# Optimization experiments

Measured on AMD Instinct MI355X. Metric: run time of the kernel, lower is better.

The kernel has to match this reference:

```python
import jax, jax.numpy as jnp
import numpy as np

E, NG, NM, H = 260640, 65160, 40962, 256


def _layer_norm(x, g, b, eps=1e-5):
    mu = jnp.mean(x, axis=-1, keepdims=True)
    var = jnp.mean(jnp.square(x - mu), axis=-1, keepdims=True)
    return (x - mu) * jax.lax.rsqrt(var + eps) * g + b


def _mlp(x, W1, b1, W2, b2, g, b):
    # Linear -> SiLU -> Linear -> LayerNorm (MLP with n_layers=1)
    h = jax.nn.silu(x @ W1 + b1)
    return _layer_norm(h @ W2 + b2, g, b)


def _lin(key, fan_in, fan_out):
    kw, kb = jax.random.split(key)
    s = 1.0 / np.sqrt(fan_in)
    W = jax.random.uniform(kw, (fan_in, fan_out), jnp.float32, -s, s)
    bb = jax.random.uniform(kb, (fan_out,), jnp.float32, -s, s)
    return W, bb


def setup_inputs() -> dict:
    key = jax.random.key(0)
    ks = jax.random.split(key, 12)
    inp = {
        'g2m_efeat': jax.random.normal(ks[0], (E, H), jnp.float32),
        'grid_feat': jax.random.normal(ks[1], (NG, H), jnp.float32),
        'mesh_feat': jax.random.normal(ks[2], (NM, H), jnp.float32),
        'src_idx': jax.random.randint(ks[3], (E,), 0, NG),
        'dst_idx': jax.random.randint(ks[4], (E,), 0, NM),
    }
    # edge MLP: in = 3H (efeat + src + dst)
    inp['eW1'], inp['eb1'] = _lin(ks[5], 3 * H, H)
    inp['eW2'], inp['eb2'] = _lin(ks[6], H, H)
    inp['eg'], inp['ebt'] = jnp.ones((H,), jnp.float32), jnp.zeros((H,), jnp.float32)
    # src (grid) node MLP: in = H
    inp['sW1'], inp['sb1'] = _lin(ks[7], H, H)
    inp['sW2'], inp['sb2'] = _lin(ks[8], H, H)
    inp['sg'], inp['sbt'] = jnp.ones((H,), jnp.float32), jnp.zeros((H,), jnp.float32)
    # dst (mesh) node MLP: in = 2H (agg + mesh)
    inp['dW1'], inp['db1'] = _lin(ks[9], 2 * H, H)
    inp['dW2'], inp['db2'] = _lin(ks[10], H, H)
    inp['dg'], inp['dbt'] = jnp.ones((H,), jnp.float32), jnp.zeros((H,), jnp.float32)
    return inp


def reference(g2m_efeat, grid_feat, mesh_feat, src_idx, dst_idx,
              eW1, eb1, eW2, eb2, eg, ebt,
              sW1, sb1, sW2, sb2, sg, sbt,
              dW1, db1, dW2, db2, dg, dbt):
    # gather src/dst node features and concat with edge features  [E, 3H]
    cat = jnp.concatenate([g2m_efeat, grid_feat[src_idx], mesh_feat[dst_idx]], axis=-1)
    efeat = _mlp(cat, eW1, eb1, eW2, eb2, eg, ebt)  # [E, H]
    # scatter-sum edges to mesh (dst) nodes, concat with mesh feats
    agg = jax.ops.segment_sum(efeat, dst_idx, num_segments=mesh_feat.shape[0])  # [NM, H]
    mesh_new = mesh_feat + _mlp(jnp.concatenate([agg, mesh_feat], axis=-1),
                                dW1, db1, dW2, db2, dg, dbt)
    grid_new = grid_feat + _mlp(grid_feat, sW1, sb1, sW2, sb2, sg, sbt)
    return (grid_new, mesh_new)
```

## Files before the change

### kernel.cpp

```cpp
#include <hip/hip_runtime.h>

#define Hdim 256
static const int E_N  = 260640;
static const int NG_N = 65160;
static const int NM_N = 40962;

typedef __attribute__((ext_vector_type(8))) __bf16 bf16x8;
typedef __attribute__((ext_vector_type(8))) unsigned short u16x8;
typedef __attribute__((ext_vector_type(4))) float f32x4;

__device__ __forceinline__ unsigned short f2bf(float f) {
  unsigned u = __float_as_uint(f);
  u = (u + 0x7FFFu + ((u >> 16) & 1u)) >> 16;
  return (unsigned short)u;
}
__device__ __forceinline__ float bf2f(unsigned short h) {
  return __uint_as_float((unsigned)h << 16);
}
struct BfPair { unsigned short hi, lo; };
__device__ __forceinline__ BfPair split2(float f) {
  BfPair r;
  r.hi = f2bf(f);
  r.lo = f2bf(f - bf2f(r.hi));
  return r;
}
__device__ __forceinline__ BfPair split2t(float f) {
  unsigned u = __float_as_uint(f);
  BfPair r;
  r.hi = (unsigned short)(u >> 16);
  r.lo = f2bf(f - __uint_as_float(u & 0xffff0000u));
  return r;
}
__device__ __forceinline__ int hswz(int row) {
  return ((row & 7) << 3) ^ (((row >> 2) & 3) << 4);
}
__device__ __forceinline__ void bar_lds() {
  asm volatile("s_waitcnt lgkmcnt(0)" ::: "memory");
  __builtin_amdgcn_s_barrier();
}

__global__ void wfrag_kernel(const float* __restrict__ W,
                             unsigned short* __restrict__ Fh,
                             unsigned short* __restrict__ Fl, int K, int N) {
  int i = blockIdx.x * 256 + threadIdx.x;
  if (i >= K * N) return;
  int k = i / N;
  int col = i - k * N;
  BfPair p = split2(W[i]);
  int t = k >> 5, rem = k & 31;
  int lg = rem >> 3, j = rem & 7;
  int cb = col >> 4, lr = col & 15;
  long o = ((long)(t * 16 + cb) * 64 + (lg * 16 + lr)) * 8 + j;
  Fh[o] = p.hi;
  Fl[o] = p.lo;
}

template <bool A3>
struct SMem {
  union {
    unsigned short ahi[2][64][72];
    float lnp[4][64][2];
  } u;
  unsigned short alo[A3 ? 2 : 1][A3 ? 64 : 1][A3 ? 72 : 1];
  unsigned short hh[64 * 256];
};

template <int NSEG, bool SCATTER, bool A3>
__launch_bounds__(256, 2)
__global__ void mlp_mfma(
    const float* s0, const float* s1, const float* s2,
    const int* __restrict__ i1, const int* __restrict__ i2, int M,
    const unsigned short* __restrict__ W1Fh, const unsigned short* __restrict__ W1Fl,
    const float* __restrict__ b1,
    const unsigned short* __restrict__ W2Fh, const unsigned short* __restrict__ W2Fl,
    const float* __restrict__ b2,
    const float* __restrict__ gamma, const float* __restrict__ beta,
    const float* residual, float* outp,
    float* agg, const int* __restrict__ scat) {
  constexpr int K1 = NSEG * 256;
  constexpr int NT = K1 / 32;
  constexpr int NU = K1 / 64;
  __shared__ SMem<A3> sm;

  const int tid = threadIdx.x;
  const int w = tid >> 6;
  const int l = tid & 63;
  const int lr = l & 15;
  const int lg = l >> 4;
  const int colbase = w * 64 + lr;
  const long blockRow = (long)blockIdx.x * 64;

  const long grow_s = blockRow + l;
  const long growc = grow_s < M ? grow_s : (long)(M - 1);
  const float* rp0 = s0 + growc * Hdim;
  const float* rp1 = nullptr;
  const float* rp2 = nullptr;
  if (NSEG >= 2) rp1 = s1 + (long)(i1 ? i1[growc] : (int)growc) * Hdim;
  if (NSEG >= 3) rp2 = s2 + (long)(i2 ? i2[growc] : (int)growc) * Hdim;

  auto aptr = [&](int m) -> const float* {
    const int seg = m >> 2;
    const float* rp = rp0;
    if (NSEG >= 2 && seg == 1) rp = rp1;
    if (NSEG >= 3 && seg == 2) rp = rp2;
    return rp + (m & 3) * 64 + w * 16;
  };

  auto loadA = [&](int m, float4* v) {
    const float* p = aptr(m);
#pragma unroll
    for (int i = 0; i < 4; ++i) v[i] = *(const float4*)(p + i * 4);
  };

  auto stageA = [&](int buf, const float4* v) {
    float in[16] = {v[0].x, v[0].y, v[0].z, v[0].w, v[1].x, v[1].y, v[1].z, v[1].w,
                    v[2].x, v[2].y, v[2].z, v[2].w, v[3].x, v[3].y, v[3].z, v[3].w};
    if constexpr (A3) {
      u16x8 th0, tl0, th1, tl1;
#pragma unroll
      for (int j = 0; j < 8; ++j) {
        BfPair p0 = split2t(in[j]);
        th0[j] = p0.hi; tl0[j] = p0.lo;
        BfPair p1 = split2t(in[j + 8]);
        th1[j] = p1.hi; tl1[j] = p1.lo;
      }
      *(u16x8*)&sm.u.ahi[buf][l][w * 16]     = th0;
      *(u16x8*)&sm.u.ahi[buf][l][w * 16 + 8] = th1;
      *(u16x8*)&sm.alo[buf][l][w * 16]       = tl0;
      *(u16x8*)&sm.alo[buf][l][w * 16 + 8]   = tl1;
    } else {
      u16x8 th0, th1;
#pragma unroll
      for (int j = 0; j < 8; ++j) {
        th0[j] = f2bf(in[j]);
        th1[j] = f2bf(in[j + 8]);
      }
      *(u16x8*)&sm.u.ahi[buf][l][w * 16]     = th0;
      *(u16x8*)&sm.u.ahi[buf][l][w * 16 + 8] = th1;
    }
  };

  auto loadB1 = [&](int t, bf16x8* bh, bf16x8* bl) {
#pragma unroll
    for (int n = 0; n < 4; ++n) {
      const long o = ((long)(t * 16 + w * 4 + n) * 64 + l) * 8;
      bh[n] = *(const bf16x8*)(W1Fh + o);
      bl[n] = *(const bf16x8*)(W1Fl + o);
    }
  };

  f32x4 acc[4][4] = {};
  {
    float4 v[4];
    loadA(0, v);
    stageA(0, v);
  }
  float4 va[4], vb[4];
  loadA(1 < NU ? 1 : NU - 1, va);
  bf16x8 bhc[4], blc[4];
  loadB1(0, bhc, blc);

  for (int u = 0; u < NU; ++u) {
    bar_lds();
    loadA(u + 2 < NU ? u + 2 : NU - 1, vb);
    bf16x8 bhn[4], bln[4];
    loadB1(2 * u + 1 < NT ? 2 * u + 1 : NT - 1, bhn, bln);
    bf16x8 ah[4], al[4];
#pragma unroll
    for (int rb = 0; rb < 4; ++rb) {
      ah[rb] = *(const bf16x8*)&sm.u.ahi[u & 1][rb * 16 + lr][lg * 8];
      if constexpr (A3) al[rb] = *(const bf16x8*)&sm.alo[u & 1][rb * 16 + lr][lg * 8];
    }
    __builtin_amdgcn_s_setprio(1);
#pragma unroll
    for (int rb = 0; rb < 4; ++rb)
#pragma unroll
      for (int n = 0; n < 4; ++n) {
        acc[rb][n] = __builtin_amdgcn_mfma_f32_16x16x32_bf16(ah[rb], bhc[n], acc[rb][n], 0, 0, 0);
        acc[rb][n] = __builtin_amdgcn_mfma_f32_16x16x32_bf16(ah[rb], blc[n], acc[rb][n], 0, 0, 0);
        if constexpr (A3)
          acc[rb][n] = __builtin_amdgcn_mfma_f32_16x16x32_bf16(al[rb], bhc[n], acc[rb][n], 0, 0, 0);
      }
    __builtin_amdgcn_s_setprio(0);
    bf16x8 bh2[4], bl2[4];
    loadB1(2 * u + 2 < NT ? 2 * u + 2 : NT - 1, bh2, bl2);
#pragma unroll
    for (int rb = 0; rb < 4; ++rb) {
      ah[rb] = *(const bf16x8*)&sm.u.ahi[u & 1][rb * 16 + lr][32 + lg * 8];
      if constexpr (A3) al[rb] = *(const bf16x8*)&sm.alo[u & 1][rb * 16 + lr][32 + lg * 8];
    }
    __builtin_amdgcn_s_setprio(1);
#pragma unroll
    for (int rb = 0; rb < 4; ++rb)
#pragma unroll
      for (int n = 0; n < 4; ++n) {
        acc[rb][n] = __builtin_amdgcn_mfma_f32_16x16x32_bf16(ah[rb], bhn[n], acc[rb][n], 0, 0, 0);
        acc[rb][n] = __builtin_amdgcn_mfma_f32_16x16x32_bf16(ah[rb], bln[n], acc[rb][n], 0, 0, 0);
        if constexpr (A3)
          acc[rb][n] = __builtin_amdgcn_mfma_f32_16x16x32_bf16(al[rb], bhn[n], acc[rb][n], 0, 0, 0);
      }
    __builtin_amdgcn_s_setprio(0);
    if (u + 1 < NU) stageA((u + 1) & 1, va);
#pragma unroll
    for (int i = 0; i < 4; ++i) va[i] = vb[i];
#pragma unroll
    for (int n = 0; n < 4; ++n) { bhc[n] = bh2[n]; blc[n] = bl2[n]; }
  }

  bf16x8 b2hc[4], b2lc[4];
#pragma unroll
  for (int n = 0; n < 4; ++n) {
    const long o = ((long)(w * 4 + n) * 64 + l) * 8;
    b2hc[n] = *(const bf16x8*)(W2Fh + o);
    b2lc[n] = *(const bf16x8*)(W2Fl + o);
  }

  float bb1[4];
#pragma unroll
  for (int n = 0; n < 4; ++n) bb1[n] = b1[colbase + n * 16];
#pragma unroll
  for (int rb = 0; rb < 4; ++rb) {
#pragma unroll
    for (int n = 0; n < 4; ++n) {
      const int col = colbase + n * 16;
#pragma unroll
      for (int r = 0; r < 4; ++r) {
        const int row = rb * 16 + lg * 4 + r;
        float v = acc[rb][n][r] + bb1[n];
        v = v / (1.0f + __expf(-v));
        sm.hh[row * 256 + (col ^ hswz(row))] = f2bf(v);
      }
    }
  }
  bar_lds();

  f32x4 acc2[4][4] = {};
  for (int ks = 0; ks < 8; ++ks) {
    const int kn = (ks + 1 < 8) ? ks + 1 : ks;
    bf16x8 b2hn[4], b2ln[4];
#pragma unroll
    for (int n = 0; n < 4; ++n) {
      const long o = ((long)(kn * 16 + w * 4 + n) * 64 + l) * 8;
      b2hn[n] = *(const bf16x8*)(W2Fh + o);
      b2ln[n] = *(const bf16x8*)(W2Fl + o);
    }
    bf16x8 ah[4];
#pragma unroll
    for (int rb = 0; rb < 4; ++rb) {
      const int row = rb * 16 + lr;
      ah[rb] = *(const bf16x8*)&sm.hh[row * 256 + ((ks * 32 + lg * 8) ^ hswz(row))];
    }
    __builtin_amdgcn_s_setprio(1);
#pragma unroll
    for (int rb = 0; rb < 4; ++rb)
#pragma unroll
      for (int n = 0; n < 4; ++n) {
        acc2[rb][n] = __builtin_amdgcn_mfma_f32_16x16x32_bf16(ah[rb], b2hc[n], acc2[rb][n], 0, 0, 0);
        acc2[rb][n] = __builtin_amdgcn_mfma_f32_16x16x32_bf16(ah[rb], b2lc[n], acc2[rb][n], 0, 0, 0);
      }
    __builtin_amdgcn_s_setprio(0);
#pragma unroll
    for (int n = 0; n < 4; ++n) { b2hc[n] = b2hn[n]; b2lc[n] = b2ln[n]; }
  }
  __syncthreads();

  float bb2[4], gmv[4], btv[4];
#pragma unroll
  for (int n = 0; n < 4; ++n) {
    const int c = colbase + n * 16;
    bb2[n] = b2[c];
    gmv[n] = gamma[c];
    btv[n] = beta[c];
  }
  float psum[16];
#pragma unroll
  for (int rb = 0; rb < 4; ++rb)
#pragma unroll
    for (int r = 0; r < 4; ++r) {
      float s = 0.f;
#pragma unroll
      for (int n = 0; n < 4; ++n) s += acc2[rb][n][r] + bb2[n];
      psum[rb * 4 + r] = s;
    }
#pragma unroll
  for (int i = 0; i < 16; ++i) {
    psum[i] += __shfl_xor(psum[i], 1, 64);
    psum[i] += __shfl_xor(psum[i], 2, 64);
    psum[i] += __shfl_xor(psum[i], 4, 64);
    psum[i] += __shfl_xor(psum[i], 8, 64);
  }
  if (lr == 0) {
#pragma unroll
    for (int rb = 0; rb < 4; ++rb)
#pragma unroll
      for (int r = 0; r < 4; ++r)
        sm.u.lnp[w][rb * 16 + lg * 4 + r][0] = psum[rb * 4 + r];
  }
  __syncthreads();
  float mu[16];
#pragma unroll
  for (int rb = 0; rb < 4; ++rb)
#pragma unroll
    for (int r = 0; r < 4; ++r) {
      const int row = rb * 16 + lg * 4 + r;
      mu[rb * 4 + r] = (sm.u.lnp[0][row][0] + sm.u.lnp[1][row][0] +
                        sm.u.lnp[2][row][0] + sm.u.lnp[3][row][0]) * (1.0f / 256.0f);
    }
  float psq[16];
#pragma unroll
  for (int rb = 0; rb < 4; ++rb)
#pragma unroll
    for (int r = 0; r < 4; ++r) {
      float s = 0.f;
#pragma unroll
      for (int n = 0; n < 4; ++n) {
        const float d = acc2[rb][n][r] + bb2[n] - mu[rb * 4 + r];
        s += d * d;
      }
      psq[rb * 4 + r] = s;
    }
#pragma unroll
  for (int i = 0; i < 16; ++i) {
    psq[i] += __shfl_xor(psq[i], 1, 64);
    psq[i] += __shfl_xor(psq[i], 2, 64);
    psq[i] += __shfl_xor(psq[i], 4, 64);
    psq[i] += __shfl_xor(psq[i], 8, 64);
  }
  if (lr == 0) {
#pragma unroll
    for (int rb = 0; rb < 4; ++rb)
#pragma unroll
      for (int r = 0; r < 4; ++r)
        sm.u.lnp[w][rb * 16 + lg * 4 + r][1] = psq[rb * 4 + r];
  }
  __syncthreads();
#pragma unroll
  for (int rb = 0; rb < 4; ++rb) {
#pragma unroll
    for (int r = 0; r < 4; ++r) {
      const int row = rb * 16 + lg * 4 + r;
      const long grow = blockRow + row;
      if (grow >= M) continue;
      const float var = (sm.u.lnp[0][row][1] + sm.u.lnp[1][row][1] +
                         sm.u.lnp[2][row][1] + sm.u.lnp[3][row][1]) * (1.0f / 256.0f);
      const float rstd = 1.0f / sqrtf(var + 1e-5f);
      const float m = mu[rb * 4 + r];
      if constexpr (SCATTER) {
        const int d = scat[grow];
        float* ap = agg + (long)d * Hdim;
#pragma unroll
        for (int n = 0; n < 4; ++n) {
          const int c = colbase + n * 16;
          atomicAdd(ap + c, (acc2[rb][n][r] + bb2[n] - m) * rstd * gmv[n] + btv[n]);
        }
      } else {
        const long o = grow * Hdim;
#pragma unroll
        for (int n = 0; n < 4; ++n) {
          const int c = colbase + n * 16;
          outp[o + c] = (acc2[rb][n][r] + bb2[n] - m) * rstd * gmv[n] + btv[n] + residual[o + c];
        }
      }
    }
  }
}

extern "C" void kernel_launch(void* const* d_in, const int* in_sizes, int n_in,
                              void* d_out, int out_size, void* d_ws, size_t ws_size,
                              hipStream_t stream) {
  const float* g2m   = (const float*)d_in[0];
  const float* gridf = (const float*)d_in[1];
  const float* meshf = (const float*)d_in[2];
  const int*   src   = (const int*)d_in[3];
  const int*   dst   = (const int*)d_in[4];
  const float* eW1 = (const float*)d_in[5];  const float* eb1 = (const float*)d_in[6];
  const float* eW2 = (const float*)d_in[7];  const float* eb2 = (const float*)d_in[8];
  const float* eg  = (const float*)d_in[9];  const float* ebt = (const float*)d_in[10];
  const float* sW1 = (const float*)d_in[11]; const float* sb1 = (const float*)d_in[12];
  const float* sW2 = (const float*)d_in[13]; const float* sb2 = (const float*)d_in[14];
  const float* sg  = (const float*)d_in[15]; const float* sbt = (const float*)d_in[16];
  const float* dW1 = (const float*)d_in[17]; const float* db1 = (const float*)d_in[18];
  const float* dW2 = (const float*)d_in[19]; const float* db2 = (const float*)d_in[20];
  const float* dg  = (const float*)d_in[21]; const float* dbt = (const float*)d_in[22];

  float* out_grid = (float*)d_out;
  float* out_mesh = out_grid + (long)NG_N * Hdim;

  unsigned short* p = (unsigned short*)d_ws;
  unsigned short* eW1Fh = p; p += 768 * 256;  unsigned short* eW1Fl = p; p += 768 * 256;
  unsigned short* eW2Fh = p; p += 256 * 256;  unsigned short* eW2Fl = p; p += 256 * 256;
  unsigned short* sW1Fh = p; p += 256 * 256;  unsigned short* sW1Fl = p; p += 256 * 256;
  unsigned short* sW2Fh = p; p += 256 * 256;  unsigned short* sW2Fl = p; p += 256 * 256;
  unsigned short* dW1Fh = p; p += 512 * 256;  unsigned short* dW1Fl = p; p += 512 * 256;
  unsigned short* dW2Fh = p; p += 256 * 256;  unsigned short* dW2Fl = p; p += 256 * 256;

  auto WF = [&](const float* W, unsigned short* Fh, unsigned short* Fl, int K, int N) {
    int tot = K * N;
    wfrag_kernel<<<(tot + 255) / 256, 256, 0, stream>>>(W, Fh, Fl, K, N);
  };
  WF(eW1, eW1Fh, eW1Fl, 768, 256);
  WF(eW2, eW2Fh, eW2Fl, 256, 256);
  WF(sW1, sW1Fh, sW1Fl, 256, 256);
  WF(sW2, sW2Fh, sW2Fl, 256, 256);
  WF(dW1, dW1Fh, dW1Fl, 512, 256);
  WF(dW2, dW2Fh, dW2Fl, 256, 256);

  (void)hipMemsetAsync(out_mesh, 0, (size_t)NM_N * Hdim * sizeof(float), stream);

  mlp_mfma<3, true, false><<<(E_N + 63) / 64, 256, 0, stream>>>(
      g2m, gridf, meshf, src, dst, E_N,
      eW1Fh, eW1Fl, eb1, eW2Fh, eW2Fl, eb2, eg, ebt,
      nullptr, nullptr, out_mesh, dst);

  mlp_mfma<1, false, true><<<(NG_N + 63) / 64, 256, 0, stream>>>(
      gridf, nullptr, nullptr, nullptr, nullptr, NG_N,
      sW1Fh, sW1Fl, sb1, sW2Fh, sW2Fl, sb2, sg, sbt,
      gridf, out_grid, nullptr, nullptr);

  mlp_mfma<2, false, true><<<(NM_N + 63) / 64, 256, 0, stream>>>(
      out_mesh, meshf, nullptr, nullptr, nullptr, NM_N,
      dW1Fh, dW1Fl, db1, dW2Fh, dW2Fl, db2, dg, dbt,
      meshf, out_mesh, nullptr, nullptr);
}
```

Measured before the change: 752.9 us.

## Split MLP block across eight waves with half the output columns each

Raises the block from 256 to 512 threads so each of eight waves computes 32 output columns instead of 64, halving per-wave accumulator and B-fragment registers. A-tile staging is spread over eight waves and the LayerNorm partial sums now reduce over eight wave slots. This is meant to raise waves per CU and improve latency hiding. In exchange, each wave rereads the full A fragments from LDS for half the MFMA work, and barriers now synchronise more waves.

```diff
diff --git a/kernel.cpp b/kernel.cpp
--- a/kernel.cpp
+++ b/kernel.cpp
@@ -59,14 +59,14 @@
 struct SMem {
   union {
     unsigned short ahi[2][64][72];
-    float lnp[4][64][2];
+    float lnp[8][64][2];
   } u;
   unsigned short alo[A3 ? 2 : 1][A3 ? 64 : 1][A3 ? 72 : 1];
   unsigned short hh[64 * 256];
 };
 
 template <int NSEG, bool SCATTER, bool A3>
-__launch_bounds__(256, 2)
+__launch_bounds__(512, 2)
 __global__ void mlp_mfma(
     const float* s0, const float* s1, const float* s2,
     const int* __restrict__ i1, const int* __restrict__ i2, int M,
@@ -87,7 +87,7 @@
   const int l = tid & 63;
   const int lr = l & 15;
   const int lg = l >> 4;
-  const int colbase = w * 64 + lr;
+  const int colbase = w * 32 + lr;
   const long blockRow = (long)blockIdx.x * 64;
 
   const long grow_s = blockRow + l;
@@ -103,67 +103,58 @@
     const float* rp = rp0;
     if (NSEG >= 2 && seg == 1) rp = rp1;
     if (NSEG >= 3 && seg == 2) rp = rp2;
-    return rp + (m & 3) * 64 + w * 16;
+    return rp + (m & 3) * 64 + w * 8;
   };
 
   auto loadA = [&](int m, float4* v) {
     const float* p = aptr(m);
-#pragma unroll
-    for (int i = 0; i < 4; ++i) v[i] = *(const float4*)(p + i * 4);
+    v[0] = *(const float4*)p;
+    v[1] = *(const float4*)(p + 4);
   };
 
   auto stageA = [&](int buf, const float4* v) {
-    float in[16] = {v[0].x, v[0].y, v[0].z, v[0].w, v[1].x, v[1].y, v[1].z, v[1].w,
-                    v[2].x, v[2].y, v[2].z, v[2].w, v[3].x, v[3].y, v[3].z, v[3].w};
+    float in[8] = {v[0].x, v[0].y, v[0].z, v[0].w, v[1].x, v[1].y, v[1].z, v[1].w};
     if constexpr (A3) {
-      u16x8 th0, tl0, th1, tl1;
+      u16x8 th, tl;
 #pragma unroll
       for (int j = 0; j < 8; ++j) {
         BfPair p0 = split2t(in[j]);
-        th0[j] = p0.hi; tl0[j] = p0.lo;
-        BfPair p1 = split2t(in[j + 8]);
-        th1[j] = p1.hi; tl1[j] = p1.lo;
-      }
-      *(u16x8*)&sm.u.ahi[buf][l][w * 16]     = th0;
-      *(u16x8*)&sm.u.ahi[buf][l][w * 16 + 8] = th1;
-      *(u16x8*)&sm.alo[buf][l][w * 16]       = tl0;
-      *(u16x8*)&sm.alo[buf][l][w * 16 + 8]   = tl1;
+        th[j] = p0.hi; tl[j] = p0.lo;
+      }
+      *(u16x8*)&sm.u.ahi[buf][l][w * 8] = th;
+      *(u16x8*)&sm.alo[buf][l][w * 8]   = tl;
     } else {
-      u16x8 th0, th1;
-#pragma unroll
-      for (int j = 0; j < 8; ++j) {
-        th0[j] = f2bf(in[j]);
-        th1[j] = f2bf(in[j + 8]);
-      }
-      *(u16x8*)&sm.u.ahi[buf][l][w * 16]     = th0;
-      *(u16x8*)&sm.u.ahi[buf][l][w * 16 + 8] = th1;
+      u16x8 th;
+#pragma unroll
+      for (int j = 0; j < 8; ++j) th[j] = f2bf(in[j]);
+      *(u16x8*)&sm.u.ahi[buf][l][w * 8] = th;
     }
   };
 
   auto loadB1 = [&](int t, bf16x8* bh, bf16x8* bl) {
 #pragma unroll
-    for (int n = 0; n < 4; ++n) {
-      const long o = ((long)(t * 16 + w * 4 + n) * 64 + l) * 8;
+    for (int n = 0; n < 2; ++n) {
+      const long o = ((long)(t * 16 + w * 2 + n) * 64 + l) * 8;
       bh[n] = *(const bf16x8*)(W1Fh + o);
       bl[n] = *(const bf16x8*)(W1Fl + o);
     }
   };
 
-  f32x4 acc[4][4] = {};
+  f32x4 acc[4][2] = {};
   {
-    float4 v[4];
+    float4 v[2];
     loadA(0, v);
     stageA(0, v);
   }
-  float4 va[4], vb[4];
+  float4 va[2], vb[2];
   loadA(1 < NU ? 1 : NU - 1, va);
-  bf16x8 bhc[4], blc[4];
+  bf16x8 bhc[2], blc[2];
   loadB1(0, bhc, blc);
 
   for (int u = 0; u < NU; ++u) {
     bar_lds();
     loadA(u + 2 < NU ? u + 2 : NU - 1, vb);
-    bf16x8 bhn[4], bln[4];
+    bf16x8 bhn[2], bln[2];
     loadB1(2 * u + 1 < NT ? 2 * u + 1 : NT - 1, bhn, bln);
     bf16x8 ah[4], al[4];
 #pragma unroll
@@ -175,14 +166,14 @@
 #pragma unroll
     for (int rb = 0; rb < 4; ++rb)
 #pragma unroll
-      for (int n = 0; n < 4; ++n) {
+      for (int n = 0; n < 2; ++n) {
         acc[rb][n] = __builtin_amdgcn_mfma_f32_16x16x32_bf16(ah[rb], bhc[n], acc[rb][n], 0, 0, 0);
         acc[rb][n] = __builtin_amdgcn_mfma_f32_16x16x32_bf16(ah[rb], blc[n], acc[rb][n], 0, 0, 0);
         if constexpr (A3)
           acc[rb][n] = __builtin_amdgcn_mfma_f32_16x16x32_bf16(al[rb], bhc[n], acc[rb][n], 0, 0, 0);
       }
     __builtin_amdgcn_s_setprio(0);
-    bf16x8 bh2[4], bl2[4];
+    bf16x8 bh2[2], bl2[2];
     loadB1(2 * u + 2 < NT ? 2 * u + 2 : NT - 1, bh2, bl2);
 #pragma unroll
     for (int rb = 0; rb < 4; ++rb) {
@@ -193,7 +184,7 @@
 #pragma unroll
     for (int rb = 0; rb < 4; ++rb)
 #pragma unroll
-      for (int n = 0; n < 4; ++n) {
+      for (int n = 0; n < 2; ++n) {
         acc[rb][n] = __builtin_amdgcn_mfma_f32_16x16x32_bf16(ah[rb], bhn[n], acc[rb][n], 0, 0, 0);
         acc[rb][n] = __builtin_amdgcn_mfma_f32_16x16x32_bf16(ah[rb], bln[n], acc[rb][n], 0, 0, 0);
         if constexpr (A3)
@@ -202,26 +193,26 @@
     __builtin_amdgcn_s_setprio(0);
     if (u + 1 < NU) stageA((u + 1) & 1, va);
 #pragma unroll
-    for (int i = 0; i < 4; ++i) va[i] = vb[i];
-#pragma unroll
-    for (int n = 0; n < 4; ++n) { bhc[n] = bh2[n]; blc[n] = bl2[n]; }
-  }
-
-  bf16x8 b2hc[4], b2lc[4];
-#pragma unroll
-  for (int n = 0; n < 4; ++n) {
-    const long o = ((long)(w * 4 + n) * 64 + l) * 8;
+    for (int i = 0; i < 2; ++i) va[i] = vb[i];
+#pragma unroll
+    for (int n = 0; n < 2; ++n) { bhc[n] = bh2[n]; blc[n] = bl2[n]; }
+  }
+
+  bf16x8 b2hc[2], b2lc[2];
+#pragma unroll
+  for (int n = 0; n < 2; ++n) {
+    const long o = ((long)(w * 2 + n) * 64 + l) * 8;
     b2hc[n] = *(const bf16x8*)(W2Fh + o);
     b2lc[n] = *(const bf16x8*)(W2Fl + o);
   }
 
-  float bb1[4];
-#pragma unroll
-  for (int n = 0; n < 4; ++n) bb1[n] = b1[colbase + n * 16];
+  float bb1[2];
+#pragma unroll
+  for (int n = 0; n < 2; ++n) bb1[n] = b1[colbase + n * 16];
 #pragma unroll
   for (int rb = 0; rb < 4; ++rb) {
 #pragma unroll
-    for (int n = 0; n < 4; ++n) {
+    for (int n = 0; n < 2; ++n) {
       const int col = colbase + n * 16;
 #pragma unroll
       for (int r = 0; r < 4; ++r) {
@@ -234,13 +225,13 @@
   }
   bar_lds();
 
-  f32x4 acc2[4][4] = {};
+  f32x4 acc2[4][2] = {};
   for (int ks = 0; ks < 8; ++ks) {
     const int kn = (ks + 1 < 8) ? ks + 1 : ks;
-    bf16x8 b2hn[4], b2ln[4];
-#pragma unroll
-    for (int n = 0; n < 4; ++n) {
-      const long o = ((long)(kn * 16 + w * 4 + n) * 64 + l) * 8;
+    bf16x8 b2hn[2], b2ln[2];
+#pragma unroll
+    for (int n = 0; n < 2; ++n) {
+      const long o = ((long)(kn * 16 + w * 2 + n) * 64 + l) * 8;
       b2hn[n] = *(const bf16x8*)(W2Fh + o);
       b2ln[n] = *(const bf16x8*)(W2Fl + o);
     }
@@ -254,19 +245,19 @@
 #pragma unroll
     for (int rb = 0; rb < 4; ++rb)
 #pragma unroll
-      for (int n = 0; n < 4; ++n) {
+      for (int n = 0; n < 2; ++n) {
         acc2[rb][n] = __builtin_amdgcn_mfma_f32_16x16x32_bf16(ah[rb], b2hc[n], acc2[rb][n], 0, 0, 0);
         acc2[rb][n] = __builtin_amdgcn_mfma_f32_16x16x32_bf16(ah[rb], b2lc[n], acc2[rb][n], 0, 0, 0);
       }
     __builtin_amdgcn_s_setprio(0);
 #pragma unroll
-    for (int n = 0; n < 4; ++n) { b2hc[n] = b2hn[n]; b2lc[n] = b2ln[n]; }
+    for (int n = 0; n < 2; ++n) { b2hc[n] = b2hn[n]; b2lc[n] = b2ln[n]; }
   }
   __syncthreads();
 
-  float bb2[4], gmv[4], btv[4];
-#pragma unroll
-  for (int n = 0; n < 4; ++n) {
+  float bb2[2], gmv[2], btv[2];
+#pragma unroll
+  for (int n = 0; n < 2; ++n) {
     const int c = colbase + n * 16;
     bb2[n] = b2[c];
     gmv[n] = gamma[c];
@@ -279,7 +270,7 @@
     for (int r = 0; r < 4; ++r) {
       float s = 0.f;
 #pragma unroll
-      for (int n = 0; n < 4; ++n) s += acc2[rb][n][r] + bb2[n];
+      for (int n = 0; n < 2; ++n) s += acc2[rb][n][r] + bb2[n];
       psum[rb * 4 + r] = s;
     }
 #pragma unroll
@@ -303,8 +294,10 @@
 #pragma unroll
     for (int r = 0; r < 4; ++r) {
       const int row = rb * 16 + lg * 4 + r;
-      mu[rb * 4 + r] = (sm.u.lnp[0][row][0] + sm.u.lnp[1][row][0] +
-                        sm.u.lnp[2][row][0] + sm.u.lnp[3][row][0]) * (1.0f / 256.0f);
+      float s = 0.f;
+#pragma unroll
+      for (int q = 0; q < 8; ++q) s += sm.u.lnp[q][row][0];
+      mu[rb * 4 + r] = s * (1.0f / 256.0f);
     }
   float psq[16];
 #pragma unroll
@@ -313,7 +306,7 @@
     for (int r = 0; r < 4; ++r) {
       float s = 0.f;
 #pragma unroll
-      for (int n = 0; n < 4; ++n) {
+      for (int n = 0; n < 2; ++n) {
         const float d = acc2[rb][n][r] + bb2[n] - mu[rb * 4 + r];
         s += d * d;
       }
@@ -341,22 +334,24 @@
       const int row = rb * 16 + lg * 4 + r;
       const long grow = blockRow + row;
       if (grow >= M) continue;
-      const float var = (sm.u.lnp[0][row][1] + sm.u.lnp[1][row][1] +
-                         sm.u.lnp[2][row][1] + sm.u.lnp[3][row][1]) * (1.0f / 256.0f);
+      float sq = 0.f;
+#pragma unroll
+      for (int q = 0; q < 8; ++q) sq += sm.u.lnp[q][row][1];
+      const float var = sq * (1.0f / 256.0f);
       const float rstd = 1.0f / sqrtf(var + 1e-5f);
       const float m = mu[rb * 4 + r];
       if constexpr (SCATTER) {
         const int d = scat[grow];
         float* ap = agg + (long)d * Hdim;
 #pragma unroll
-        for (int n = 0; n < 4; ++n) {
+        for (int n = 0; n < 2; ++n) {
           const int c = colbase + n * 16;
           atomicAdd(ap + c, (acc2[rb][n][r] + bb2[n] - m) * rstd * gmv[n] + btv[n]);
         }
       } else {
         const long o = grow * Hdim;
 #pragma unroll
-        for (int n = 0; n < 4; ++n) {
+        for (int n = 0; n < 2; ++n) {
           const int c = colbase + n * 16;
           outp[o + c] = (acc2[rb][n][r] + bb2[n] - m) * rstd * gmv[n] + btv[n] + residual[o + c];
         }
@@ -407,17 +402,17 @@
 
   (void)hipMemsetAsync(out_mesh, 0, (size_t)NM_N * Hdim * sizeof(float), stream);
 
-  mlp_mfma<3, true, false><<<(E_N + 63) / 64, 256, 0, stream>>>(
+  mlp_mfma<3, true, false><<<(E_N + 63) / 64, 512, 0, stream>>>(
       g2m, gridf, meshf, src, dst, E_N,
       eW1Fh, eW1Fl, eb1, eW2Fh, eW2Fl, eb2, eg, ebt,
       nullptr, nullptr, out_mesh, dst);
 
-  mlp_mfma<1, false, true><<<(NG_N + 63) / 64, 256, 0, stream>>>(
+  mlp_mfma<1, false, true><<<(NG_N + 63) / 64, 512, 0, stream>>>(
       gridf, nullptr, nullptr, nullptr, nullptr, NG_N,
       sW1Fh, sW1Fl, sb1, sW2Fh, sW2Fl, sb2, sg, sbt,
       gridf, out_grid, nullptr, nullptr);
 
-  mlp_mfma<2, false, true><<<(NM_N + 63) / 64, 256, 0, stream>>>(
+  mlp_mfma<2, false, true><<<(NM_N + 63) / 64, 512, 0, stream>>>(
       out_mesh, meshf, nullptr, nullptr, nullptr, NM_N,
       dW1Fh, dW1Fl, db1, dW2Fh, dW2Fl, db2, dg, dbt,
       meshf, out_mesh, nullptr, nullptr);
```

New measurement: 982.9 us (median of 2 runs). 1.31x slower.

## Split edge MLP into gather-to-bf16-fragment pass and 128-row register-fed GEMM kernel

Applied to the files above, without the earlier changes.

The edge MLP is split into two kernels. The first gathers the concatenated edge/src/dst features, converts them to bf16, and writes them to a workspace buffer already laid out in MFMA fragment order. The second kernel uses 512 threads on 128-row tiles and loads A fragments straight from global memory into registers, skipping LDS staging and per-iteration barriers in the first GEMM. The cost is an extra round trip of roughly 400MB of bf16 through global memory, along with larger register use per thread.

```diff
diff --git a/kernel.cpp b/kernel.cpp
--- a/kernel.cpp
+++ b/kernel.cpp
@@ -4,6 +4,9 @@
 static const int E_N  = 260640;
 static const int NG_N = 65160;
 static const int NM_N = 40962;
+static const int NB_E = (E_N + 127) / 128;
+static const int RT_N = NB_E * 8;
+static const int GB_N = RT_N / 4;
 
 typedef __attribute__((ext_vector_type(8))) __bf16 bf16x8;
 typedef __attribute__((ext_vector_type(8))) unsigned short u16x8;
@@ -55,32 +58,290 @@
   Fl[o] = p.lo;
 }
 
+__global__ __launch_bounds__(256, 4)
+void gather_frag(const float* __restrict__ g2m, const float* __restrict__ gridf,
+                 const float* __restrict__ meshf, const int* __restrict__ src,
+                 const int* __restrict__ dst, int M,
+                 unsigned short* __restrict__ catF) {
+  __shared__ unsigned short tile[64][72];
+  const int tid = threadIdx.x;
+  const int w = tid >> 6;
+  const int l = tid & 63;
+  const int lr = l & 15;
+  const int lg = l >> 4;
+  const long blockRow = (long)blockIdx.x * 64;
+  long growc = blockRow + l;
+  if (growc >= M) growc = M - 1;
+  const float* rp0 = g2m + growc * Hdim;
+  const float* rp1 = gridf + (long)src[growc] * Hdim;
+  const float* rp2 = meshf + (long)dst[growc] * Hdim;
+
+  for (int m = 0; m < 12; ++m) {
+    const int seg = m >> 2;
+    const float* rp = seg == 0 ? rp0 : (seg == 1 ? rp1 : rp2);
+    const float* p = rp + (m & 3) * 64 + w * 16;
+    float4 v0 = *(const float4*)p;
+    float4 v1 = *(const float4*)(p + 4);
+    float4 v2 = *(const float4*)(p + 8);
+    float4 v3 = *(const float4*)(p + 12);
+    __syncthreads();
+    {
+      float in[16] = {v0.x, v0.y, v0.z, v0.w, v1.x, v1.y, v1.z, v1.w,
+                      v2.x, v2.y, v2.z, v2.w, v3.x, v3.y, v3.z, v3.w};
+      u16x8 t0, t1;
+#pragma unroll
+      for (int j = 0; j < 8; ++j) {
+        t0[j] = f2bf(in[j]);
+        t1[j] = f2bf(in[j + 8]);
+      }
+      *(u16x8*)&tile[l][w * 16]     = t0;
+      *(u16x8*)&tile[l][w * 16 + 8] = t1;
+    }
+    __syncthreads();
+    const long rowtile = (long)blockIdx.x * 4 + w;
+#pragma unroll
+    for (int tt = 0; tt < 2; ++tt) {
+      const int t = m * 2 + tt;
+      u16x8 v = *(const u16x8*)&tile[w * 16 + lr][tt * 32 + lg * 8];
+      *(u16x8*)&catF[((rowtile * 24 + t) * 64 + l) * 8] = v;
+    }
+  }
+}
+
+struct ESMem {
+  unsigned short hh[128 * 256];
+  float lnp[8][128][2];
+};
+
+__global__ __launch_bounds__(512, 2)
+void edge_gemm(const unsigned short* __restrict__ catF, int M,
+               const unsigned short* __restrict__ W1Fh, const unsigned short* __restrict__ W1Fl,
+               const float* __restrict__ b1,
+               const unsigned short* __restrict__ W2Fh, const unsigned short* __restrict__ W2Fl,
+               const float* __restrict__ b2,
+               const float* __restrict__ gamma, const float* __restrict__ beta,
+               float* __restrict__ agg, const int* __restrict__ scat) {
+  __shared__ ESMem sm;
+  const int tid = threadIdx.x;
+  const int w = tid >> 6;
+  const int l = tid & 63;
+  const int lr = l & 15;
+  const int lg = l >> 4;
+  const int colbase = w * 32 + lr;
+  const long blockRow = (long)blockIdx.x * 128;
+  const long rt0 = (long)blockIdx.x * 8;
+
+  auto loadAF = [&](int t, bf16x8* af) {
+#pragma unroll
+    for (int rb = 0; rb < 8; ++rb)
+      af[rb] = *(const bf16x8*)(catF + (((rt0 + rb) * 24 + t) * 64 + l) * 8);
+  };
+  auto loadB1 = [&](int t, bf16x8* bh, bf16x8* bl) {
+#pragma unroll
+    for (int n = 0; n < 2; ++n) {
+      const long o = ((long)(t * 16 + w * 2 + n) * 64 + l) * 8;
+      bh[n] = *(const bf16x8*)(W1Fh + o);
+      bl[n] = *(const bf16x8*)(W1Fl + o);
+    }
+  };
+
+  f32x4 acc[8][2] = {};
+  bf16x8 afc[8], afn[8], bhc[2], blc[2], bhn[2], bln[2];
+  loadAF(0, afc);
+  loadB1(0, bhc, blc);
+  for (int t = 0; t < 24; ++t) {
+    const int tn = t + 1 < 24 ? t + 1 : 23;
+    loadAF(tn, afn);
+    loadB1(tn, bhn, bln);
+    __builtin_amdgcn_s_setprio(1);
+#pragma unroll
+    for (int rb = 0; rb < 8; ++rb)
+#pragma unroll
+      for (int n = 0; n < 2; ++n) {
+        acc[rb][n] = __builtin_amdgcn_mfma_f32_16x16x32_bf16(afc[rb], bhc[n], acc[rb][n], 0, 0, 0);
+        acc[rb][n] = __builtin_amdgcn_mfma_f32_16x16x32_bf16(afc[rb], blc[n], acc[rb][n], 0, 0, 0);
+      }
+    __builtin_amdgcn_s_setprio(0);
+#pragma unroll
+    for (int rb = 0; rb < 8; ++rb) afc[rb] = afn[rb];
+#pragma unroll
+    for (int n = 0; n < 2; ++n) { bhc[n] = bhn[n]; blc[n] = bln[n]; }
+  }
+
+  bf16x8 b2hc[2], b2lc[2];
+#pragma unroll
+  for (int n = 0; n < 2; ++n) {
+    const long o = ((long)(w * 2 + n) * 64 + l) * 8;
+    b2hc[n] = *(const bf16x8*)(W2Fh + o);
+    b2lc[n] = *(const bf16x8*)(W2Fl + o);
+  }
+
+  float bb1[2];
+#pragma unroll
+  for (int n = 0; n < 2; ++n) bb1[n] = b1[colbase + n * 16];
+#pragma unroll
+  for (int rb = 0; rb < 8; ++rb) {
+#pragma unroll
+    for (int n = 0; n < 2; ++n) {
+      const int col = colbase + n * 16;
+#pragma unroll
+      for (int r = 0; r < 4; ++r) {
+        const int row = rb * 16 + lg * 4 + r;
+        float v = acc[rb][n][r] + bb1[n];
+        v = v / (1.0f + __expf(-v));
+        sm.hh[row * 256 + (col ^ hswz(row))] = f2bf(v);
+      }
+    }
+  }
+  bar_lds();
+
+  f32x4 acc2[8][2] = {};
+  for (int ks = 0; ks < 8; ++ks) {
+    const int kn = (ks + 1 < 8) ? ks + 1 : ks;
+    bf16x8 b2hn[2], b2ln[2];
+#pragma unroll
+    for (int n = 0; n < 2; ++n) {
+      const long o = ((long)(kn * 16 + w * 2 + n) * 64 + l) * 8;
+      b2hn[n] = *(const bf16x8*)(W2Fh + o);
+      b2ln[n] = *(const bf16x8*)(W2Fl + o);
+    }
+    __builtin_amdgcn_s_setprio(1);
+#pragma unroll
+    for (int rb = 0; rb < 8; ++rb) {
+      const int row = rb * 16 + lr;
+      bf16x8 ah = *(const bf16x8*)&sm.hh[row * 256 + ((ks * 32 + lg * 8) ^ hswz(row))];
+#pragma unroll
+      for (int n = 0; n < 2; ++n) {
+        acc2[rb][n] = __builtin_amdgcn_mfma_f32_16x16x32_bf16(ah, b2hc[n], acc2[rb][n], 0, 0, 0);
+        acc2[rb][n] = __builtin_amdgcn_mfma_f32_16x16x32_bf16(ah, b2lc[n], acc2[rb][n], 0, 0, 0);
+      }
+    }
+    __builtin_amdgcn_s_setprio(0);
+#pragma unroll
+    for (int n = 0; n < 2; ++n) { b2hc[n] = b2hn[n]; b2lc[n] = b2ln[n]; }
+  }
+
+  float bb2[2], gmv[2], btv[2];
+#pragma unroll
+  for (int n = 0; n < 2; ++n) {
+    const int c = colbase + n * 16;
+    bb2[n] = b2[c];
+    gmv[n] = gamma[c];
+    btv[n] = beta[c];
+  }
+  float psum[32];
+#pragma unroll
+  for (int rb = 0; rb < 8; ++rb)
+#pragma unroll
+    for (int r = 0; r < 4; ++r) {
+      float s = 0.f;
+#pragma unroll
+      for (int n = 0; n < 2; ++n) s += acc2[rb][n][r] + bb2[n];
+      psum[rb * 4 + r] = s;
+    }
+#pragma unroll
+  for (int i = 0; i < 32; ++i) {
+    psum[i] += __shfl_xor(psum[i], 1, 64);
+    psum[i] += __shfl_xor(psum[i], 2, 64);
+    psum[i] += __shfl_xor(psum[i], 4, 64);
+    psum[i] += __shfl_xor(psum[i], 8, 64);
+  }
+  if (lr == 0) {
+#pragma unroll
+    for (int rb = 0; rb < 8; ++rb)
+#pragma unroll
+      for (int r = 0; r < 4; ++r)
+        sm.lnp[w][rb * 16 + lg * 4 + r][0] = psum[rb * 4 + r];
+  }
+  __syncthreads();
+  float mu[32];
+#pragma unroll
+  for (int rb = 0; rb < 8; ++rb)
+#pragma unroll
+    for (int r = 0; r < 4; ++r) {
+      const int row = rb * 16 + lg * 4 + r;
+      float s = 0.f;
+#pragma unroll
+      for (int q = 0; q < 8; ++q) s += sm.lnp[q][row][0];
+      mu[rb * 4 + r] = s * (1.0f / 256.0f);
+    }
+  float psq[32];
+#pragma unroll
+  for (int rb = 0; rb < 8; ++rb)
+#pragma unroll
+    for (int r = 0; r < 4; ++r) {
+      float s = 0.f;
+#pragma unroll
+      for (int n = 0; n < 2; ++n) {
+        const float d = acc2[rb][n][r] + bb2[n] - mu[rb * 4 + r];
+        s += d * d;
+      }
+      psq[rb * 4 + r] = s;
+    }
+#pragma unroll
+  for (int i = 0; i < 32; ++i) {
+    psq[i] += __shfl_xor(psq[i], 1, 64);
+    psq[i] += __shfl_xor(psq[i], 2, 64);
+    psq[i] += __shfl_xor(psq[i], 4, 64);
+    psq[i] += __shfl_xor(psq[i], 8, 64);
+  }
+  if (lr == 0) {
+#pragma unroll
+    for (int rb = 0; rb < 8; ++rb)
+#pragma unroll
+      for (int r = 0; r < 4; ++r)
+        sm.lnp[w][rb * 16 + lg * 4 + r][1] = psq[rb * 4 + r];
+  }
+  __syncthreads();
+#pragma unroll
+  for (int rb = 0; rb < 8; ++rb) {
+#pragma unroll
+    for (int r = 0; r < 4; ++r) {
+      const int row = rb * 16 + lg * 4 + r;
+      const long grow = blockRow + row;
+      if (grow >= M) continue;
+      float sq = 0.f;
+#pragma unroll
+      for (int q = 0; q < 8; ++q) sq += sm.lnp[q][row][1];
+      const float var = sq * (1.0f / 256.0f);
+      const float rstd = 1.0f / sqrtf(var + 1e-5f);
+      const float m = mu[rb * 4 + r];
+      const int d = scat[grow];
+      float* ap = agg + (long)d * Hdim;
+#pragma unroll
+      for (int n = 0; n < 2; ++n) {
+        const int c = colbase + n * 16;
+        atomicAdd(ap + c, (acc2[rb][n][r] + bb2[n] - m) * rstd * gmv[n] + btv[n]);
+      }
+    }
+  }
+}
+
 template <bool A3>
 struct SMem {
   union {
     unsigned short ahi[2][64][72];
     float lnp[4][64][2];
   } u;
-  unsigned short alo[A3 ? 2 : 1][A3 ? 64 : 1][A3 ? 72 : 1];
+  unsigned short alo[2][64][72];
   unsigned short hh[64 * 256];
 };
 
-template <int NSEG, bool SCATTER, bool A3>
+template <int NSEG>
 __launch_bounds__(256, 2)
 __global__ void mlp_mfma(
-    const float* s0, const float* s1, const float* s2,
-    const int* __restrict__ i1, const int* __restrict__ i2, int M,
+    const float* s0, const float* s1,
+    const int* __restrict__ i1, int M,
     const unsigned short* __restrict__ W1Fh, const unsigned short* __restrict__ W1Fl,
     const float* __restrict__ b1,
     const unsigned short* __restrict__ W2Fh, const unsigned short* __restrict__ W2Fl,
     const float* __restrict__ b2,
     const float* __restrict__ gamma, const float* __restrict__ beta,
-    const float* residual, float* outp,
-    float* agg, const int* __restrict__ scat) {
+    const float* residual, float* outp) {
   constexpr int K1 = NSEG * 256;
   constexpr int NT = K1 / 32;
   constexpr int NU = K1 / 64;
-  __shared__ SMem<A3> sm;
+  __shared__ SMem<true> sm;
 
   const int tid = threadIdx.x;
   const int w = tid >> 6;
@@ -94,52 +355,34 @@
   const long growc = grow_s < M ? grow_s : (long)(M - 1);
   const float* rp0 = s0 + growc * Hdim;
   const float* rp1 = nullptr;
-  const float* rp2 = nullptr;
   if (NSEG >= 2) rp1 = s1 + (long)(i1 ? i1[growc] : (int)growc) * Hdim;
-  if (NSEG >= 3) rp2 = s2 + (long)(i2 ? i2[growc] : (int)growc) * Hdim;
 
   auto aptr = [&](int m) -> const float* {
     const int seg = m >> 2;
-    const float* rp = rp0;
-    if (NSEG >= 2 && seg == 1) rp = rp1;
-    if (NSEG >= 3 && seg == 2) rp = rp2;
+    const float* rp = (NSEG >= 2 && seg == 1) ? rp1 : rp0;
     return rp + (m & 3) * 64 + w * 16;
   };
-
   auto loadA = [&](int m, float4* v) {
     const float* p = aptr(m);
 #pragma unroll
     for (int i = 0; i < 4; ++i) v[i] = *(const float4*)(p + i * 4);
   };
-
   auto stageA = [&](int buf, const float4* v) {
     float in[16] = {v[0].x, v[0].y, v[0].z, v[0].w, v[1].x, v[1].y, v[1].z, v[1].w,
                     v[2].x, v[2].y, v[2].z, v[2].w, v[3].x, v[3].y, v[3].z, v[3].w};
-    if constexpr (A3) {
-      u16x8 th0, tl0, th1, tl1;
-#pragma unroll
-      for (int j = 0; j < 8; ++j) {
-        BfPair p0 = split2t(in[j]);
-        th0[j] = p0.hi; tl0[j] = p0.lo;
-        BfPair p1 = split2t(in[j + 8]);
-        th1[j] = p1.hi; tl1[j] = p1.lo;
-      }
-      *(u16x8*)&sm.u.ahi[buf][l][w * 16]     = th0;
-      *(u16x8*)&sm.u.ahi[buf][l][w * 16 + 8] = th1;
-      *(u16x8*)&sm.alo[buf][l][w * 16]       = tl0;
-      *(u16x8*)&sm.alo[buf][l][w * 16 + 8]   = tl1;
-    } else {
-      u16x8 th0, th1;
-#pragma unroll
-      for (int j = 0; j < 8; ++j) {
-        th0[j] = f2bf(in[j]);
-        th1[j] = f2bf(in[j + 8]);
-      }
-      *(u16x8*)&sm.u.ahi[buf][l][w * 16]     = th0;
-      *(u16x8*)&sm.u.ahi[buf][l][w * 16 + 8] = th1;
-    }
+    u16x8 th0, tl0, th1, tl1;
+#pragma unroll
+    for (int j = 0; j < 8; ++j) {
+      BfPair p0 = split2t(in[j]);
+      th0[j] = p0.hi; tl0[j] = p0.lo;
+      BfPair p1 = split2t(in[j + 8]);
+      th1[j] = p1.hi; tl1[j] = p1.lo;
+    }
+    *(u16x8*)&sm.u.ahi[buf][l][w * 16]     = th0;
+    *(u16x8*)&sm.u.ahi[buf][l][w * 16 + 8] = th1;
+    *(u16x8*)&sm.alo[buf][l][w * 16]       = tl0;
+    *(u16x8*)&sm.alo[buf][l][w * 16 + 8]   = tl1;
   };
-
   auto loadB1 = [&](int t, bf16x8* bh, bf16x8* bl) {
 #pragma unroll
     for (int n = 0; n < 4; ++n) {
@@ -169,7 +412,7 @@
 #pragma unroll
     for (int rb = 0; rb < 4; ++rb) {
       ah[rb] = *(const bf16x8*)&sm.u.ahi[u & 1][rb * 16 + lr][lg * 8];
-      if constexpr (A3) al[rb] = *(const bf16x8*)&sm.alo[u & 1][rb * 16 + lr][lg * 8];
+      al[rb] = *(const bf16x8*)&sm.alo[u & 1][rb * 16 + lr][lg * 8];
     }
     __builtin_amdgcn_s_setprio(1);
 #pragma unroll
@@ -178,8 +421,7 @@
       for (int n = 0; n < 4; ++n) {
         acc[rb][n] = __builtin_amdgcn_mfma_f32_16x16x32_bf16(ah[rb], bhc[n], acc[rb][n], 0, 0, 0);
         acc[rb][n] = __builtin_amdgcn_mfma_f32_16x16x32_bf16(ah[rb], blc[n], acc[rb][n], 0, 0, 0);
-        if constexpr (A3)
-          acc[rb][n] = __builtin_amdgcn_mfma_f32_16x16x32_bf16(al[rb], bhc[n], acc[rb][n], 0, 0, 0);
+        acc[rb][n] = __builtin_amdgcn_mfma_f32_16x16x32_bf16(al[rb], bhc[n], acc[rb][n], 0, 0, 0);
       }
     __builtin_amdgcn_s_setprio(0);
     bf16x8 bh2[4], bl2[4];
@@ -187,7 +429,7 @@
 #pragma unroll
     for (int rb = 0; rb < 4; ++rb) {
       ah[rb] = *(const bf16x8*)&sm.u.ahi[u & 1][rb * 16 + lr][32 + lg * 8];
-      if constexpr (A3) al[rb] = *(const bf16x8*)&sm.alo[u & 1][rb * 16 + lr][32 + lg * 8];
+      al[rb] = *(const bf16x8*)&sm.alo[u & 1][rb * 16 + lr][32 + lg * 8];
     }
     __builtin_amdgcn_s_setprio(1);
 #pragma unroll
@@ -196,8 +438,7 @@
       for (int n = 0; n < 4; ++n) {
         acc[rb][n] = __builtin_amdgcn_mfma_f32_16x16x32_bf16(ah[rb], bhn[n], acc[rb][n], 0, 0, 0);
         acc[rb][n] = __builtin_amdgcn_mfma_f32_16x16x32_bf16(ah[rb], bln[n], acc[rb][n], 0, 0, 0);
-        if constexpr (A3)
-          acc[rb][n] = __builtin_amdgcn_mfma_f32_16x16x32_bf16(al[rb], bhn[n], acc[rb][n], 0, 0, 0);
+        acc[rb][n] = __builtin_amdgcn_mfma_f32_16x16x32_bf16(al[rb], bhn[n], acc[rb][n], 0, 0, 0);
       }
     __builtin_amdgcn_s_setprio(0);
     if (u + 1 < NU) stageA((u + 1) & 1, va);
@@ -345,21 +586,11 @@
                          sm.u.lnp[2][row][1] + sm.u.lnp[3][row][1]) * (1.0f / 256.0f);
       const float rstd = 1.0f / sqrtf(var + 1e-5f);
       const float m = mu[rb * 4 + r];
-      if constexpr (SCATTER) {
-        const int d = scat[grow];
-        float* ap = agg + (long)d * Hdim;
-#pragma unroll
-        for (int n = 0; n < 4; ++n) {
-          const int c = colbase + n * 16;
-          atomicAdd(ap + c, (acc2[rb][n][r] + bb2[n] - m) * rstd * gmv[n] + btv[n]);
-        }
-      } else {
-        const long o = grow * Hdim;
-#pragma unroll
-        for (int n = 0; n < 4; ++n) {
-          const int c = colbase + n * 16;
-          outp[o + c] = (acc2[rb][n][r] + bb2[n] - m) * rstd * gmv[n] + btv[n] + residual[o + c];
-        }
+      const long o = grow * Hdim;
+#pragma unroll
+      for (int n = 0; n < 4; ++n) {
+        const int c = colbase + n * 16;
+        outp[o + c] = (acc2[rb][n][r] + bb2[n] - m) * rstd * gmv[n] + btv[n] + residual[o + c];
       }
     }
   }
@@ -393,6 +624,7 @@
   unsigned short* sW2Fh = p; p += 256 * 256;  unsigned short* sW2Fl = p; p += 256 * 256;
   unsigned short* dW1Fh = p; p += 512 * 256;  unsigned short* dW1Fl = p; p += 512 * 256;
   unsigned short* dW2Fh = p; p += 256 * 256;  unsigned short* dW2Fl = p; p += 256 * 256;
+  unsigned short* catF  = p;
 
   auto WF = [&](const float* W, unsigned short* Fh, unsigned short* Fl, int K, int N) {
     int tot = K * N;
@@ -407,18 +639,18 @@
 
   (void)hipMemsetAsync(out_mesh, 0, (size_t)NM_N * Hdim * sizeof(float), stream);
 
-  mlp_mfma<3, true, false><<<(E_N + 63) / 64, 256, 0, stream>>>(
-      g2m, gridf, meshf, src, dst, E_N,
-      eW1Fh, eW1Fl, eb1, eW2Fh, eW2Fl, eb2, eg, ebt,
-      nullptr, nullptr, out_mesh, dst);
-
-  mlp_mfma<1, false, true><<<(NG_N + 63) / 64, 256, 0, stream>>>(
-      gridf, nullptr, nullptr, nullptr, nullptr, NG_N,
+  gather_frag<<<GB_N, 256, 0, stream>>>(g2m, gridf, meshf, src, dst, E_N, catF);
+
+  edge_gemm<<<NB_E, 512, 0, stream>>>(
+      catF, E_N, eW1Fh, eW1Fl, eb1, eW2Fh, eW2Fl, eb2, eg, ebt, out_mesh, dst);
+
+  mlp_mfma<1><<<(NG_N + 63) / 64, 256, 0, stream>>>(
+      gridf, nullptr, nullptr, NG_N,
       sW1Fh, sW1Fl, sb1, sW2Fh, sW2Fl, sb2, sg, sbt,
-      gridf, out_grid, nullptr, nullptr);
-
-  mlp_mfma<2, false, true><<<(NM_N + 63) / 64, 256, 0, stream>>>(
-      out_mesh, meshf, nullptr, nullptr, nullptr, NM_N,
+      gridf, out_grid);
+
+  mlp_mfma<2><<<(NM_N + 63) / 64, 256, 0, stream>>>(
+      out_mesh, meshf, nullptr, NM_N,
       dW1Fh, dW1Fl, db1, dW2Fh, dW2Fl, db2, dg, dbt,
-      meshf, out_mesh, nullptr, nullptr);
-}
+      meshf, out_mesh);
+}
```

New measurement: 0.9997 ms. 1.33x slower.
